# Optimization experiments

Measured on AMD Instinct MI355X. Metric: run time of the kernel, lower is better.

The kernel has to match this reference:

```python
import jax, jax.numpy as jnp
import numpy as np

HILBERT_BITS = 8
NDIM = 3


def hilbert_distance(grid, bits=HILBERT_BITS):
    """Vectorized Skilling transform: grid [..., 3] int32 in [0, 2**bits-1] -> Hilbert index [...] int32.
    Exact port of hilbertcurve.HilbertCurve.distance_from_point (n=3, p=bits)."""
    x = [grid[..., i] for i in range(NDIM)]
    m = 1 << (bits - 1)
    # Inverse undo excess work
    q = m
    while q > 1:
        pm = q - 1
        for i in range(NDIM):
            cond = (x[i] & q) != 0
            if i == 0:
                x[0] = jnp.where(cond, x[0] ^ pm, x[0])
            else:
                t = (x[0] ^ x[i]) & pm
                x0n = jnp.where(cond, x[0] ^ pm, x[0] ^ t)
                xin = jnp.where(cond, x[i], x[i] ^ t)
                x[0], x[i] = x0n, xin
        q >>= 1
    # Gray encode
    x[1] = x[1] ^ x[0]
    x[2] = x[2] ^ x[1]
    t = jnp.zeros_like(x[2])
    q = m
    while q > 1:
        t = jnp.where((x[2] & q) != 0, t ^ (q - 1), t)
        q >>= 1
    x = [xi ^ t for xi in x]
    # Interleave bits, MSB first, dim order 0,1,2 -> h has bits*3 bits (24 fits int32)
    h = jnp.zeros_like(x[0])
    for bpos in range(bits - 1, -1, -1):
        for i in range(NDIM):
            h = (h << 1) | ((x[i] >> bpos) & 1)
    return h


def hilbert_orders(x, bits=HILBERT_BITS):
    # x: [B, N, 3] float. Per-batch min/max normalization, then quantize to grid.
    mins = x.min(axis=1, keepdims=True)
    maxs = x.max(axis=1, keepdims=True)
    span = jnp.maximum(maxs - mins, 1e-6)
    norm = (x - mins) / span
    mx = (1 << bits) - 1
    grid_h = jnp.clip(norm * mx, 0, mx).astype(jnp.int32)
    grid_t = jnp.clip(norm[..., ::-1] * mx, 0, mx).astype(jnp.int32)  # [z,y,x] variant
    order_h = jnp.argsort(hilbert_distance(grid_h, bits), axis=-1)
    order_t = jnp.argsort(hilbert_distance(grid_t, bits), axis=-1)
    return order_h, order_t


def setup_inputs() -> dict:
    key = jax.random.key(0)
    k1, k2, k3 = jax.random.split(key, 3)
    B, N, D = 16, 4096, 384
    x = jax.random.normal(k1, (B, N, 3), dtype=jnp.float32)
    W = jax.random.normal(k2, (D, 3), dtype=jnp.float32) * 0.5
    b = jax.random.normal(k3, (D,), dtype=jnp.float32) * 0.1
    gamma = jnp.ones((2, D), dtype=jnp.float32)
    beta = jnp.zeros((2, D), dtype=jnp.float32)
    return {"x": x, "W": W, "b": b, "gamma": gamma, "beta": beta}


def reference(x, W, b, gamma, beta):
    order_h, order_t = hilbert_orders(x)                     # [B, N] each
    pts_h = jnp.take_along_axis(x, order_h[..., None], axis=1)  # [B, N, 3]
    pts_t = jnp.take_along_axis(x, order_t[..., None], axis=1)
    base_h = jnp.einsum('bnc,dc->bnd', pts_h, W) + b         # Linear(3, D)
    base_t = jnp.einsum('bnc,dc->bnd', pts_t, W) + b
    tokens_h = base_h * gamma[0] + beta[0]
    tokens_t = base_t * gamma[1] + beta[1]
    return jnp.concatenate([tokens_h, tokens_t], axis=1)     # [B, 2N, D]
```

## Files before the change

### kernel.cpp

```cpp
#include <hip/hip_runtime.h>
#include <stdint.h>

#define BATCH 16
#define NPTS 4096
#define DIM 384
#define NTOK (2*NPTS)
#define F4PT (DIM/4)

typedef unsigned long long u64;

__device__ __forceinline__ uint32_t spread3(uint32_t x) {
    x = (x | (x << 8)) & 0x00F00Fu;
    x = (x | (x << 4)) & 0x0C30C3u;
    x = (x | (x << 2)) & 0x249249u;
    return x;
}

__device__ __forceinline__ uint32_t hilbert3(uint32_t x0, uint32_t x1, uint32_t x2) {
    #pragma unroll
    for (uint32_t q = 128; q > 1; q >>= 1) {
        uint32_t pm = q - 1;
        if (x0 & q) x0 ^= pm;
        uint32_t t = (x0 ^ x1) & pm;
        if (x1 & q) { x0 ^= pm; } else { x0 ^= t; x1 ^= t; }
        t = (x0 ^ x2) & pm;
        if (x2 & q) { x0 ^= pm; } else { x0 ^= t; x2 ^= t; }
    }
    x1 ^= x0;
    x2 ^= x1;
    uint32_t t = 0;
    #pragma unroll
    for (uint32_t q = 128; q > 1; q >>= 1) { if (x2 & q) t ^= (q - 1); }
    x0 ^= t; x1 ^= t; x2 ^= t;
    return (spread3(x0) << 2) | (spread3(x1) << 1) | spread3(x2);
}

__global__ __launch_bounds__(512) void order_radix_o(const float* __restrict__ x,
                                                     uint32_t* __restrict__ segc_all,
                                                     unsigned short* __restrict__ segi_all) {
    const int bi = blockIdx.x;
    const int b = bi >> 4;
    const int v = (bi >> 3) & 1;
    const int oct = bi & 7;
    const int t = threadIdx.x;
    const int lane = t & 63;
    const int w = t >> 6;

    __shared__ uint32_t scode[512];
    __shared__ unsigned short slocal[512];
    __shared__ uint32_t hist[3 * 2048];
    __shared__ uint32_t baseArr[256];
    __shared__ uint32_t waveTot[4];
    __shared__ float red[8 * 6];

    const float* xb = x + (size_t)b * NPTS * 3;
    const float4* xb4 = (const float4*)xb;

    float mnx = 1e30f, mny = 1e30f, mnz = 1e30f;
    float mxx = -1e30f, mxy = -1e30f, mxz = -1e30f;
    #pragma unroll
    for (int h = 0; h < 2; ++h) {
        float4 q0 = xb4[h * 1536 + 3 * t + 0];
        float4 q1 = xb4[h * 1536 + 3 * t + 1];
        float4 q2 = xb4[h * 1536 + 3 * t + 2];
        float px[4] = {q0.x, q0.w, q1.z, q2.y};
        float py[4] = {q0.y, q1.x, q1.w, q2.z};
        float pz[4] = {q0.z, q1.y, q2.x, q2.w};
        #pragma unroll
        for (int r = 0; r < 4; ++r) {
            mnx = fminf(mnx, px[r]); mxx = fmaxf(mxx, px[r]);
            mny = fminf(mny, py[r]); mxy = fmaxf(mxy, py[r]);
            mnz = fminf(mnz, pz[r]); mxz = fmaxf(mxz, pz[r]);
        }
    }
    #pragma unroll
    for (int off = 32; off > 0; off >>= 1) {
        mnx = fminf(mnx, __shfl_xor(mnx, off));
        mny = fminf(mny, __shfl_xor(mny, off));
        mnz = fminf(mnz, __shfl_xor(mnz, off));
        mxx = fmaxf(mxx, __shfl_xor(mxx, off));
        mxy = fmaxf(mxy, __shfl_xor(mxy, off));
        mxz = fmaxf(mxz, __shfl_xor(mxz, off));
    }
    if (lane == 0) {
        red[w*6+0] = mnx; red[w*6+1] = mny; red[w*6+2] = mnz;
        red[w*6+3] = mxx; red[w*6+4] = mxy; red[w*6+5] = mxz;
    }
    #pragma unroll
    for (int c = 0; c < 12; ++c) hist[t + c * 512] = 0u;
    __syncthreads();
    if (t == 0) {
        for (int ww = 1; ww < 8; ++ww) {
            mnx = fminf(mnx, red[ww*6+0]); mny = fminf(mny, red[ww*6+1]);
            mnz = fminf(mnz, red[ww*6+2]); mxx = fmaxf(mxx, red[ww*6+3]);
            mxy = fmaxf(mxy, red[ww*6+4]); mxz = fmaxf(mxz, red[ww*6+5]);
        }
        red[0] = mnx; red[1] = mny; red[2] = mnz;
        red[3] = fmaxf(mxx - mnx, 1e-6f);
        red[4] = fmaxf(mxy - mny, 1e-6f);
        red[5] = fmaxf(mxz - mnz, 1e-6f);
    }
    __syncthreads();
    mnx = red[0]; mny = red[1]; mnz = red[2];
    const float spx = red[3], spy = red[4], spz = red[5];

    uint32_t code;
    unsigned short myidx;
    {
        const int n0 = (oct << 9) + t;
        float cx = xb[3*n0+0], cy = xb[3*n0+1], cz = xb[3*n0+2];
        float gx = fminf(fmaxf(((cx - mnx) / spx) * 255.0f, 0.0f), 255.0f);
        float gy = fminf(fmaxf(((cy - mny) / spy) * 255.0f, 0.0f), 255.0f);
        float gz = fminf(fmaxf(((cz - mnz) / spz) * 255.0f, 0.0f), 255.0f);
        uint32_t ix = (uint32_t)(int)gx;
        uint32_t iy = (uint32_t)(int)gy;
        uint32_t iz = (uint32_t)(int)gz;
        uint32_t a0 = v ? iz : ix;
        uint32_t a2 = v ? ix : iz;
        code = hilbert3(a0, iy, a2);
        myidx = (unsigned short)n0;
    }

    const u64 below_mask = (1ull << lane) - 1ull;
    uint32_t* segc = segc_all + (((b << 1) | v) << 12);
    unsigned short* segi = segi_all + (((b << 1) | v) << 12);

    #pragma unroll
    for (int p = 0; p < 3; ++p) {
        const int sh = 8 * p;
        uint32_t* histp = hist + p * 2048;

        unsigned d = (code >> sh) & 255u;
        u64 m = ~0ull;
        #pragma unroll
        for (int bit = 0; bit < 8; ++bit) {
            u64 bal = __ballot((int)((d >> bit) & 1u));
            m &= ((d >> bit) & 1u) ? bal : ~bal;
        }
        unsigned rk = (unsigned)__popcll(m & below_mask);
        if (rk == 0u)
            histp[d * 8 + w] = (unsigned)__popcll(m);
        __syncthreads();

        unsigned exclw = 0;
        if (t < 256) {
            uint32_t* hb = histp + t * 8;
            unsigned running = 0;
            #pragma unroll
            for (int s = 0; s < 8; ++s) {
                unsigned hv = hb[s];
                hb[s] = running;
                running += hv;
            }
            unsigned incl = running;
            #pragma unroll
            for (int off = 1; off < 64; off <<= 1) {
                unsigned nv = __shfl_up(incl, off);
                if (lane >= off) incl += nv;
            }
            if (lane == 63) waveTot[w] = incl;
            exclw = incl - running;
        }
        __syncthreads();

        if (t < 256) {
            unsigned base = exclw;
            #pragma unroll
            for (int ww = 0; ww < 4; ++ww)
                if (ww < w) base += waveTot[ww];
            baseArr[t] = base;
        }
        __syncthreads();

        unsigned pos = baseArr[d] + histp[d * 8 + w] + rk;

        if (p < 2) {
            scode[pos] = code;
            slocal[pos] = myidx;
            __syncthreads();
            code = scode[t];
            myidx = slocal[t];
        } else {
            segc[(oct << 9) + pos] = code;
            segi[(oct << 9) + pos] = myidx;
        }
    }
}

__global__ __launch_bounds__(512) void merge_emit_kernel(const float* __restrict__ x,
                                                         const float* __restrict__ W,
                                                         const float* __restrict__ bias,
                                                         const float* __restrict__ gamma,
                                                         const float* __restrict__ beta,
                                                         const uint32_t* __restrict__ segc_all,
                                                         const unsigned short* __restrict__ segi_all,
                                                         float4* __restrict__ out4) {
    const int bi = blockIdx.x;
    const int b = bi >> 4;
    const int v = (bi >> 3) & 1;
    const int oct = bi & 7;
    const int t = threadIdx.x;

    __shared__ uint32_t runs[8 * 512];
    __shared__ __align__(16) float sw0[DIM], sw1[DIM], sw2[DIM], sc[DIM];
    __shared__ float cxs[512], cys[512], czs[512];
    __shared__ int rnk[512];

    const uint32_t* segc = segc_all + (((b << 1) | v) << 12);
    const unsigned short* segi = segi_all + (((b << 1) | v) << 12);

    uint32_t kc = segc[(oct << 9) + t];
    int idx = (int)segi[(oct << 9) + t];
    const float* p = x + (size_t)b * NPTS * 3 + idx * 3;
    float pcx = p[0], pcy = p[1], pcz = p[2];

    if (t < DIM) {
        float g = gamma[v * DIM + t];
        sw0[t] = g * W[t*3+0];
        sw1[t] = g * W[t*3+1];
        sw2[t] = g * W[t*3+2];
        sc[t]  = g * bias[t] + beta[v * DIM + t];
    }

    {
        const uint4* s4 = (const uint4*)segc;
        uint4* r4 = (uint4*)runs;
        r4[t] = s4[t];
        r4[t + 512] = s4[t + 512];
    }
    __syncthreads();

    int rank = t;
    {
        int base7[7];
        uint32_t thr7[7];
        int c[7];
        #pragma unroll
        for (int j = 0; j < 7; ++j) {
            int oq = j + (j >= oct ? 1 : 0);
            base7[j] = oq << 9;
            thr7[j] = kc + (oq < oct ? 1u : 0u);
            c[j] = 0;
        }
        #pragma unroll
        for (int step = 512; step >= 1; step >>= 1) {
            #pragma unroll
            for (int j = 0; j < 7; ++j) {
                if (c[j] + step <= 512 && runs[base7[j] + c[j] + step - 1] < thr7[j])
                    c[j] += step;
            }
        }
        #pragma unroll
        for (int j = 0; j < 7; ++j) rank += c[j];
    }

    cxs[t] = pcx; cys[t] = pcy; czs[t] = pcz;
    rnk[t] = rank;
    __syncthreads();

    const int tokbase = (b << 13) + (v << 12);
    for (int i = t; i < 512 * F4PT; i += 512) {
        int r = i / F4PT;
        int g = i - r * F4PT;
        float pxr = cxs[r], pyr = cys[r], pzr = czs[r];
        int d0 = g << 2;
        float4 w0 = *(const float4*)&sw0[d0];
        float4 w1 = *(const float4*)&sw1[d0];
        float4 w2 = *(const float4*)&sw2[d0];
        float4 cc = *(const float4*)&sc[d0];
        float4 o;
        o.x = pxr*w0.x + pyr*w1.x + pzr*w2.x + cc.x;
        o.y = pxr*w0.y + pyr*w1.y + pzr*w2.y + cc.y;
        o.z = pxr*w0.z + pyr*w1.z + pzr*w2.z + cc.z;
        o.w = pxr*w0.w + pyr*w1.w + pzr*w2.w + cc.w;
        out4[(size_t)(tokbase + rnk[r]) * F4PT + g] = o;
    }
}

extern "C" void kernel_launch(void* const* d_in, const int* in_sizes, int n_in,
                              void* d_out, int out_size, void* d_ws, size_t ws_size,
                              hipStream_t stream) {
    const float* x     = (const float*)d_in[0];
    const float* W     = (const float*)d_in[1];
    const float* bias  = (const float*)d_in[2];
    const float* gamma = (const float*)d_in[3];
    const float* beta  = (const float*)d_in[4];

    uint32_t* segc_all = (uint32_t*)d_ws;
    unsigned short* segi_all = (unsigned short*)(segc_all + 32 * 4096);

    hipLaunchKernelGGL(order_radix_o,     dim3(BATCH * 16), dim3(512), 0, stream,
                       x, segc_all, segi_all);
    hipLaunchKernelGGL(merge_emit_kernel, dim3(BATCH * 16), dim3(512), 0, stream,
                       x, W, bias, gamma, beta, segc_all, segi_all, (float4*)d_out);
}
```

Measured before the change: 49.56 us.

## Split radix sort into 16 runs of 256 per batch-view

The first kernel now sorts 16 runs of 256 points per (batch, view) using 256-thread blocks, which doubles the grid to 512 blocks and halves per-block shared memory and histogram width. The merge kernel computes each element's rank by binary searching 15 other runs of 256 instead of 7 runs of 512. This is meant to raise occupancy and parallelism in the sort stage, at the cost of more binary searches per element in the merge stage. Each sort block also now scans the whole batch's points for min/max, so that redundant read happens 32 times per batch instead of 16.

```diff
diff --git a/kernel.cpp b/kernel.cpp
--- a/kernel.cpp
+++ b/kernel.cpp
@@ -6,6 +6,8 @@
 #define DIM 384
 #define NTOK (2*NPTS)
 #define F4PT (DIM/4)
+#define NRUN 16
+#define RUN 256
 
 typedef unsigned long long u64;
 
@@ -35,23 +37,23 @@
     return (spread3(x0) << 2) | (spread3(x1) << 1) | spread3(x2);
 }
 
-__global__ __launch_bounds__(512) void order_radix_o(const float* __restrict__ x,
+__global__ __launch_bounds__(256) void order_radix_s(const float* __restrict__ x,
                                                      uint32_t* __restrict__ segc_all,
                                                      unsigned short* __restrict__ segi_all) {
     const int bi = blockIdx.x;
-    const int b = bi >> 4;
-    const int v = (bi >> 3) & 1;
-    const int oct = bi & 7;
+    const int b = bi >> 5;
+    const int v = (bi >> 4) & 1;
+    const int sed = bi & 15;
     const int t = threadIdx.x;
     const int lane = t & 63;
     const int w = t >> 6;
 
-    __shared__ uint32_t scode[512];
-    __shared__ unsigned short slocal[512];
-    __shared__ uint32_t hist[3 * 2048];
+    __shared__ uint32_t scode[RUN];
+    __shared__ unsigned short slocal[RUN];
+    __shared__ uint32_t hist[3 * 1024];
     __shared__ uint32_t baseArr[256];
     __shared__ uint32_t waveTot[4];
-    __shared__ float red[8 * 6];
+    __shared__ float red[4 * 6];
 
     const float* xb = x + (size_t)b * NPTS * 3;
     const float4* xb4 = (const float4*)xb;
@@ -59,10 +61,10 @@
     float mnx = 1e30f, mny = 1e30f, mnz = 1e30f;
     float mxx = -1e30f, mxy = -1e30f, mxz = -1e30f;
     #pragma unroll
-    for (int h = 0; h < 2; ++h) {
-        float4 q0 = xb4[h * 1536 + 3 * t + 0];
-        float4 q1 = xb4[h * 1536 + 3 * t + 1];
-        float4 q2 = xb4[h * 1536 + 3 * t + 2];
+    for (int g = 0; g < 4; ++g) {
+        float4 q0 = xb4[12*t + 3*g + 0];
+        float4 q1 = xb4[12*t + 3*g + 1];
+        float4 q2 = xb4[12*t + 3*g + 2];
         float px[4] = {q0.x, q0.w, q1.z, q2.y};
         float py[4] = {q0.y, q1.x, q1.w, q2.z};
         float pz[4] = {q0.z, q1.y, q2.x, q2.w};
@@ -87,10 +89,10 @@
         red[w*6+3] = mxx; red[w*6+4] = mxy; red[w*6+5] = mxz;
     }
     #pragma unroll
-    for (int c = 0; c < 12; ++c) hist[t + c * 512] = 0u;
+    for (int c = 0; c < 12; ++c) hist[t + c * 256] = 0u;
     __syncthreads();
     if (t == 0) {
-        for (int ww = 1; ww < 8; ++ww) {
+        for (int ww = 1; ww < 4; ++ww) {
             mnx = fminf(mnx, red[ww*6+0]); mny = fminf(mny, red[ww*6+1]);
             mnz = fminf(mnz, red[ww*6+2]); mxx = fmaxf(mxx, red[ww*6+3]);
             mxy = fmaxf(mxy, red[ww*6+4]); mxz = fmaxf(mxz, red[ww*6+5]);
@@ -107,7 +109,7 @@
     uint32_t code;
     unsigned short myidx;
     {
-        const int n0 = (oct << 9) + t;
+        const int n0 = (sed << 8) + t;
         float cx = xb[3*n0+0], cy = xb[3*n0+1], cz = xb[3*n0+2];
         float gx = fminf(fmaxf(((cx - mnx) / spx) * 255.0f, 0.0f), 255.0f);
         float gy = fminf(fmaxf(((cy - mny) / spy) * 255.0f, 0.0f), 255.0f);
@@ -128,7 +130,7 @@
     #pragma unroll
     for (int p = 0; p < 3; ++p) {
         const int sh = 8 * p;
-        uint32_t* histp = hist + p * 2048;
+        uint32_t* histp = hist + p * 1024;
 
         unsigned d = (code >> sh) & 255u;
         u64 m = ~0ull;
@@ -139,15 +141,15 @@
         }
         unsigned rk = (unsigned)__popcll(m & below_mask);
         if (rk == 0u)
-            histp[d * 8 + w] = (unsigned)__popcll(m);
+            histp[d * 4 + w] = (unsigned)__popcll(m);
         __syncthreads();
 
-        unsigned exclw = 0;
-        if (t < 256) {
-            uint32_t* hb = histp + t * 8;
+        unsigned exclw;
+        {
+            uint32_t* hb = histp + t * 4;
             unsigned running = 0;
             #pragma unroll
-            for (int s = 0; s < 8; ++s) {
+            for (int s = 0; s < 4; ++s) {
                 unsigned hv = hb[s];
                 hb[s] = running;
                 running += hv;
@@ -163,7 +165,7 @@
         }
         __syncthreads();
 
-        if (t < 256) {
+        {
             unsigned base = exclw;
             #pragma unroll
             for (int ww = 0; ww < 4; ++ww)
@@ -172,7 +174,7 @@
         }
         __syncthreads();
 
-        unsigned pos = baseArr[d] + histp[d * 8 + w] + rk;
+        unsigned pos = baseArr[d] + histp[d * 4 + w] + rk;
 
         if (p < 2) {
             scode[pos] = code;
@@ -181,8 +183,8 @@
             code = scode[t];
             myidx = slocal[t];
         } else {
-            segc[(oct << 9) + pos] = code;
-            segi[(oct << 9) + pos] = myidx;
+            segc[(sed << 8) + pos] = code;
+            segi[(sed << 8) + pos] = myidx;
         }
     }
 }
@@ -201,7 +203,7 @@
     const int oct = bi & 7;
     const int t = threadIdx.x;
 
-    __shared__ uint32_t runs[8 * 512];
+    __shared__ uint32_t runs[NRUN * RUN];
     __shared__ __align__(16) float sw0[DIM], sw1[DIM], sw2[DIM], sc[DIM];
     __shared__ float cxs[512], cys[512], czs[512];
     __shared__ int rnk[512];
@@ -209,8 +211,9 @@
     const uint32_t* segc = segc_all + (((b << 1) | v) << 12);
     const unsigned short* segi = segi_all + (((b << 1) | v) << 12);
 
-    uint32_t kc = segc[(oct << 9) + t];
-    int idx = (int)segi[(oct << 9) + t];
+    const int flat = (oct << 9) + t;
+    uint32_t kc = segc[flat];
+    int idx = (int)segi[flat];
     const float* p = x + (size_t)b * NPTS * 3 + idx * 3;
     float pcx = p[0], pcy = p[1], pcz = p[2];
 
@@ -230,28 +233,29 @@
     }
     __syncthreads();
 
-    int rank = t;
+    const int jown = flat >> 8;
+    int rank = flat & (RUN - 1);
     {
-        int base7[7];
-        uint32_t thr7[7];
-        int c[7];
-        #pragma unroll
-        for (int j = 0; j < 7; ++j) {
-            int oq = j + (j >= oct ? 1 : 0);
-            base7[j] = oq << 9;
-            thr7[j] = kc + (oq < oct ? 1u : 0u);
+        int base15[15];
+        uint32_t thr15[15];
+        int c[15];
+        #pragma unroll
+        for (int j = 0; j < 15; ++j) {
+            int oq = j + (j >= jown ? 1 : 0);
+            base15[j] = oq << 8;
+            thr15[j] = kc + (oq < jown ? 1u : 0u);
             c[j] = 0;
         }
         #pragma unroll
-        for (int step = 512; step >= 1; step >>= 1) {
+        for (int step = RUN; step >= 1; step >>= 1) {
             #pragma unroll
-            for (int j = 0; j < 7; ++j) {
-                if (c[j] + step <= 512 && runs[base7[j] + c[j] + step - 1] < thr7[j])
+            for (int j = 0; j < 15; ++j) {
+                if (c[j] + step <= RUN && runs[base15[j] + c[j] + step - 1] < thr15[j])
                     c[j] += step;
             }
         }
         #pragma unroll
-        for (int j = 0; j < 7; ++j) rank += c[j];
+        for (int j = 0; j < 15; ++j) rank += c[j];
     }
 
     cxs[t] = pcx; cys[t] = pcy; czs[t] = pcz;
@@ -289,7 +293,7 @@
     uint32_t* segc_all = (uint32_t*)d_ws;
     unsigned short* segi_all = (unsigned short*)(segc_all + 32 * 4096);
 
-    hipLaunchKernelGGL(order_radix_o,     dim3(BATCH * 16), dim3(512), 0, stream,
+    hipLaunchKernelGGL(order_radix_s,     dim3(BATCH * 32), dim3(256), 0, stream,
                        x, segc_all, segi_all);
     hipLaunchKernelGGL(merge_emit_kernel, dim3(BATCH * 16), dim3(512), 0, stream,
                        x, W, bias, gamma, beta, segc_all, segi_all, (float4*)d_out);
```

After: 54.28 us. +9.5%, slower.
